# Performance work log

Hardware: AMD Instinct MI355X
Metric: run time of the kernel (lower is better)

The kernel has to match this reference:

```python
import jax, jax.numpy as jnp
import numpy as np
import math

B = 1; SEQ = 2048; CHUNK = 16; K = SEQ // CHUNK
DIM = 1024; NH = 16; HD = DIM // NH
NL = 2; NLF = 2; HID = 4096; VOCAB = 32000; CSP_MAX = 4
EPS = 1e-5
BS = CHUNK + 2                 # per-chunk decoder block: [fx, sep, tokens]
L = K * BS + 2                 # + trailing [fx_last, sep]


def rope_cache(n_pos, n_elem, base=10000.0):
    theta = 1.0 / (base ** (jnp.arange(0, n_elem, 2, dtype=jnp.float32) / n_elem))
    idx = jnp.outer(jnp.arange(n_pos, dtype=jnp.float32), theta)  # [n_pos, n_elem/2]
    cos = jnp.concatenate([jnp.cos(idx), jnp.cos(idx)], -1)
    sin = jnp.concatenate([jnp.sin(idx), jnp.sin(idx)], -1)
    return cos, sin  # [n_pos, n_elem]


def apply_rope(x, cos, sin):
    # x: [b, h, l, d]; cos/sin: [l, d] (rope_n_elem == head_dim)
    h = x.shape[-1] // 2
    rot = jnp.concatenate([-x[..., h:], x[..., :h]], -1)
    return x * cos + rot * sin


def rmsnorm(x, w):
    return x * jax.lax.rsqrt(jnp.mean(x * x, -1, keepdims=True) + EPS) * w


def attention(x, wqkv, wo, cos, sin, mask):
    b, l, d = x.shape
    qkv = (x @ wqkv).reshape(b, l, 3, NH, HD).transpose(2, 0, 3, 1, 4)
    q, k, v = qkv[0], qkv[1], qkv[2]            # [b, h, l, hd]
    q = apply_rope(q, cos, sin)
    k = apply_rope(k, cos, sin)
    s = jnp.einsum('bhqd,bhkd->bhqk', q, k) / math.sqrt(HD)
    if mask is not None:
        s = jnp.where(mask, s, jnp.float32(-1e30))
    o = jnp.einsum('bhqk,bhkd->bhqd', jax.nn.softmax(s, -1), v)
    return o.transpose(0, 2, 1, 3).reshape(b, l, d) @ wo


def block(x, ln1, wqkv, wo, ln2, wg, wu, wd, cos, sin, mask):
    x = x + attention(rmsnorm(x, ln1), wqkv, wo, cos, sin, mask)
    h = rmsnorm(x, ln2)
    return x + (jax.nn.silu(h @ wg) * (h @ wu)) @ wd


def cat_mask(n, bs):
    # CAT mask: (kv divides block-start | same block) & causal
    q = jnp.arange(n)[:, None]
    kv = jnp.arange(n)[None, :]
    return ((kv % bs == 0) | (q // bs == kv // bs)) & (q >= kv)


def setup_inputs() -> dict:
    key = jax.random.key(0)
    ks = jax.random.split(key, 24)
    w = lambda k, s: jax.random.normal(k, s, jnp.float32) * 0.02
    return {
        'input_ids': jax.random.randint(ks[0], (B, SEQ), 0, VOCAB, dtype=jnp.int32),
        'chunk_size_power': 4,
        'f_wte': w(ks[1], (VOCAB, DIM)), 'f_pos': w(ks[2], (SEQ, DIM)),
        'f_adapt': w(ks[3], (CSP_MAX + 1, DIM)),
        'f_ln1': jnp.ones((NLF, DIM)), 'f_ln2': jnp.ones((NLF, DIM)),
        'f_wqkv': w(ks[4], (NLF, DIM, 3 * DIM)), 'f_wo': w(ks[5], (NLF, DIM, DIM)),
        'f_wg': w(ks[6], (NLF, DIM, HID)), 'f_wu': w(ks[7], (NLF, DIM, HID)),
        'f_wd': w(ks[8], (NLF, HID, DIM)),
        'f_norm': jnp.ones((DIM,)), 'f_proj': w(ks[9], (DIM, CHUNK * DIM)),
        'dummy_fx': w(ks[10], (CSP_MAX + 1, DIM)), 'wte': w(ks[11], (VOCAB, DIM)),
        'sep': w(ks[12], (1, DIM)),
        'd_ln1': jnp.ones((NL, DIM)), 'd_ln2': jnp.ones((NL, DIM)),
        'd_wqkv': w(ks[13], (NL, DIM, 3 * DIM)), 'd_wo': w(ks[14], (NL, DIM, DIM)),
        'd_wg': w(ks[15], (NL, DIM, HID)), 'd_wu': w(ks[16], (NL, DIM, HID)),
        'd_wd': w(ks[17], (NL, HID, DIM)),
        'd_norm': jnp.ones((DIM,)), 'w_out': w(ks[18], (VOCAB, DIM)),
    }


def reference(input_ids, chunk_size_power, f_wte, f_pos, f_adapt, f_ln1, f_ln2,
              f_wqkv, f_wo, f_wg, f_wu, f_wd, f_norm, f_proj, dummy_fx, wte, sep,
              d_ln1, d_ln2, d_wqkv, d_wo, d_wg, d_wu, d_wd, d_norm, w_out):
    csp = int(chunk_size_power)
    ids = input_ids.reshape(B, K, CHUNK)
    cosf, sinf = rope_cache(2 + CHUNK, HD)

    def compress(ids_c, chunk_idx):
        # ids_c: [B, CHUNK] (one chunk, vmapped over K)
        x = f_wte[ids_c]
        adaptive = jnp.broadcast_to(f_adapt[csp], (B, 1, DIM))
        pos_tok = jnp.broadcast_to(f_pos[chunk_idx], (B, 1, DIM))
        x = jnp.concatenate([adaptive, pos_tok, x], 1)  # [B, CHUNK+2, DIM]
        for i in range(NLF):
            x = block(x, f_ln1[i], f_wqkv[i], f_wo[i], f_ln2[i],
                      f_wg[i], f_wu[i], f_wd[i], cosf, sinf, None)
        x = rmsnorm(x, f_norm)[:, 2:, :].reshape(B, CHUNK * DIM)
        # chunk_size_power == log2(CHUNK): bilinear interpolate to same size == identity
        return x @ f_proj.T  # [B, DIM]

    fx = jax.vmap(compress, in_axes=(1, 0), out_axes=1)(ids, jnp.arange(K))  # [B, K, DIM]

    fx_last = fx[:, -1:, :]
    dummy = jnp.broadcast_to(dummy_fx[csp], (B, 1, DIM))
    fx_sh = jnp.concatenate([dummy, fx[:, :-1, :]], 1)[:, :, None, :]  # [B, K, 1, DIM]
    sep_t = jnp.broadcast_to(sep[0], (B, K, 1, DIM))
    emb = wte[ids]  # [B, K, CHUNK, DIM]
    x = jnp.concatenate([fx_sh, sep_t, emb], 2).reshape(B, K * BS, DIM)
    x = jnp.concatenate([x, fx_last, jnp.broadcast_to(sep[0], (B, 1, DIM))], 1)  # [B, L, DIM]

    # per-block repeating RoPE positions (cache built for len BS, tiled)
    pos = jnp.tile(jnp.arange(BS), K + 1)[:L]
    cosb, sinb = rope_cache(BS, HD)
    cosd, sind = cosb[pos], sinb[pos]
    mask = cat_mask(L, BS)

    for i in range(NL):
        x = block(x, d_ln1[i], d_wqkv[i], d_wo[i], d_ln2[i],
                  d_wg[i], d_wu[i], d_wd[i], cosd, sind, mask)
    x = rmsnorm(x, d_norm)
    return x @ w_out.T  # [B, L, VOCAB]
```

## Files before the change

### kernel.cpp

```cpp
#include <hip/hip_runtime.h>
#include <math.h>

#define L_DEC 2306
#define MPAD 2560
#define T_FINE 2304

typedef float f32x4 __attribute__((ext_vector_type(4)));
typedef __bf16 bf16x8 __attribute__((ext_vector_type(8)));
typedef unsigned short u16;
typedef unsigned short us4 __attribute__((ext_vector_type(4)));
typedef unsigned short us8 __attribute__((ext_vector_type(8)));

#define GLOAD16(g, l) __builtin_amdgcn_global_load_lds( \
    (const __attribute__((address_space(1))) unsigned int*)(g), \
    (__attribute__((address_space(3))) unsigned int*)(l), 16, 0, 0)

__device__ __forceinline__ u16 f2bf(float f) {
  unsigned u = __float_as_uint(f);
  u += 0x7fffu + ((u >> 16) & 1u);
  return (u16)(u >> 16);
}

__device__ __forceinline__ int fix_csp(const int* p) {
  int c = p[0];
  if ((unsigned)c <= 4u) return c;
  float f = __uint_as_float((unsigned)c);
  int c2 = (int)f;
  return ((unsigned)c2 <= 4u) ? c2 : 4;
}

template<int ROWMAJ>
__device__ __forceinline__ void xcd_map(int gx, int gy, int& bm, int& bn, int TS) {
  const int nwg = gx * gy;
  const int orig = blockIdx.y * gx + blockIdx.x;
  const int q8 = nwg >> 3, r8 = nwg & 7;
  const int xcd = orig & 7, idx8 = orig >> 3;
  const int wg = (xcd < r8 ? xcd * (q8 + 1) : r8 * (q8 + 1) + (xcd - r8) * q8) + idx8;
  if (ROWMAJ) { bm = (wg / gx) * TS; bn = (wg % gx) * TS; }
  else        { bm = (wg % gy) * TS; bn = (wg / gy) * TS; }
}

template<int EPI>
__global__ __launch_bounds__(512, 1) void k_gemm3(const u16* __restrict__ A,
                                                  const u16* __restrict__ B,
                                                  float* __restrict__ C,
                                                  int N, int K, int Mstore)
{
  extern __shared__ u16 lds[];
  const int tid = threadIdx.x;
  int bm, bn; xcd_map<0>(gridDim.x, gridDim.y, bm, bn, 256);
  const int w = tid >> 6, lane = tid & 63;
  const int wm = (w >> 2) * 128, wn = (w & 3) * 64;
  const int lr = lane & 15, kh = lane >> 4;

#define STAGE3(buf, kt) do {                                                   \
    u16* lA = lds + (buf) * 32768;                                             \
    u16* lB = lA + 16384;                                                      \
    _Pragma("unroll")                                                          \
    for (int p = 0; p < 4; ++p) {                                              \
      int e = p * 512 + tid;                                                   \
      int row = e >> 3;                                                        \
      int kc = ((e & 7) ^ (row & 7)) * 8;    \
      GLOAD16(A + (size_t)(bm + row) * K + (size_t)(kt) * 64 + kc, lA + e * 8);\
      GLOAD16(B + (size_t)(bn + row) * K + (size_t)(kt) * 64 + kc, lB + e * 8);\
    }                                                                          \
  } while (0)

  f32x4 acc[8][4] = {};
  const int nt = K >> 6;
  STAGE3(0, 0);
  __syncthreads();
  int cur = 0;
  for (int t = 0; t < nt; ++t) {
    if (t + 1 < nt) STAGE3(cur ^ 1, t + 1);
    const u16* pA = lds + cur * 32768;
    const u16* pB = pA + 16384;
    const int xr = (lr & 7) << 3;
#pragma unroll
    for (int kt2 = 0; kt2 < 2; ++kt2) {
      bf16x8 af[8], bf[4];
#pragma unroll
      for (int m = 0; m < 8; ++m)
        af[m] = *(const bf16x8*)&pA[(wm + m * 16 + lr) * 64 + ((kt2 * 32 + kh * 8) ^ xr)];
#pragma unroll
      for (int n = 0; n < 4; ++n)
        bf[n] = *(const bf16x8*)&pB[(wn + n * 16 + lr) * 64 + ((kt2 * 32 + kh * 8) ^ xr)];
#pragma unroll
      for (int m = 0; m < 8; ++m)
#pragma unroll
        for (int n = 0; n < 4; ++n)
          acc[m][n] = __builtin_amdgcn_mfma_f32_16x16x32_bf16(af[m], bf[n], acc[m][n], 0, 0, 0);
    }
    __syncthreads();
    cur ^= 1;
  }
#undef STAGE3

#pragma unroll
  for (int m = 0; m < 8; ++m) {
    int gr0 = bm + wm + m * 16 + kh * 4;
#pragma unroll
    for (int n = 0; n < 4; ++n) {
      int gc = bn + wn + n * 16 + lr;
#pragma unroll
      for (int r = 0; r < 4; ++r) {
        int gr = gr0 + r;
        if (gr < Mstore) C[(size_t)gr * N + gc] = acc[m][n][r];
      }
    }
  }
}

template<int EPI>
__global__ __launch_bounds__(512, 1) void k_gemm2(const u16* __restrict__ A,
                                                  const u16* __restrict__ B,
                                                  float* __restrict__ C,
                                                  u16* __restrict__ Cb,
                                                  int N, int K, int Mstore)
{
  __shared__ u16 As[2][8192];
  __shared__ u16 Bs[2][8192];
  const int tid = threadIdx.x;
  int bm, bn; xcd_map<1>(gridDim.x, gridDim.y, bm, bn, 256);
  const int w = tid >> 6, lane = tid & 63;
  const int wm = (w >> 2) * 128, wn = (w & 3) * 64;
  const int lr = lane & 15, kh = lane >> 4;
  const int r0 = tid >> 2;
  const int ksrc = 8 * ((tid & 3) ^ ((tid >> 3) & 3));
  const u16* ga = A + (size_t)(bm + r0) * K + ksrc;
  const u16* gb = B + (size_t)(bn + r0) * K + ksrc;
  const size_t rstep = (size_t)128 * K;
  const int cola = (kh * 8) ^ (((lr >> 1) & 3) << 3);

#define STAGE2(buf, kt) do {                                   \
    const u16* gA = ga + (size_t)(kt) * 32;                    \
    const u16* gB = gb + (size_t)(kt) * 32;                    \
    GLOAD16(gA,         &As[buf][tid * 8]);                    \
    GLOAD16(gA + rstep, &As[buf][tid * 8 + 4096]);             \
    GLOAD16(gB,         &Bs[buf][tid * 8]);                    \
    GLOAD16(gB + rstep, &Bs[buf][tid * 8 + 4096]);             \
  } while (0)

  f32x4 acc[8][4] = {};
  const int nt = K >> 5;
  STAGE2(0, 0);
  __syncthreads();
  int cur = 0;
  for (int t = 0; t < nt; ++t) {
    if (t + 1 < nt) STAGE2(cur ^ 1, t + 1);
    bf16x8 af[8], bf[4];
#pragma unroll
    for (int m = 0; m < 8; ++m)
      af[m] = *(const bf16x8*)&As[cur][(wm + m * 16 + lr) * 32 + cola];
#pragma unroll
    for (int n = 0; n < 4; ++n)
      bf[n] = *(const bf16x8*)&Bs[cur][(wn + n * 16 + lr) * 32 + cola];
#pragma unroll
    for (int m = 0; m < 8; ++m)
#pragma unroll
      for (int n = 0; n < 4; ++n)
        acc[m][n] = __builtin_amdgcn_mfma_f32_16x16x32_bf16(af[m], bf[n], acc[m][n], 0, 0, 0);
    __syncthreads();
    cur ^= 1;
  }
#undef STAGE2

#pragma unroll
  for (int m = 0; m < 8; ++m) {
    int gr0 = bm + wm + m * 16 + kh * 4;
#pragma unroll
    for (int n = 0; n < 4; ++n) {
      int gc = bn + wn + n * 16 + lr;
#pragma unroll
      for (int r = 0; r < 4; ++r) {
        int gr = gr0 + r;
        if (gr < Mstore) C[(size_t)gr * N + gc] = acc[m][n][r];
      }
    }
  }
}

template<int EPI>
__global__ __launch_bounds__(256) void k_gemm_bt(const u16* __restrict__ A,
                                                 const u16* __restrict__ B,
                                                 float* __restrict__ C,
                                                 u16* __restrict__ Cb,
                                                 const float* __restrict__ cosT,
                                                 const float* __restrict__ sinT,
                                                 int N, int K, int Mstore, int kchunk)
{
  __shared__ u16 As[4096];
  __shared__ u16 Bs[4096];
  const int tid = threadIdx.x;
  int bm, bn; xcd_map<1>(gridDim.x, gridDim.y, bm, bn, 128);
  const int k0 = blockIdx.z * kchunk;
  const int w = tid >> 6, lane = tid & 63;
  const int wm = (w >> 1) * 64, wn = (w & 1) * 64;
  const int lr = lane & 15, kh = lane >> 4;
  const int r0 = tid >> 2;
  const int ksrc = 8 * ((tid & 3) ^ ((tid >> 3) & 3));
  const int cola = (kh * 8) ^ (((lr >> 1) & 3) << 3);

  const u16* ga = A + (size_t)(bm + r0) * K + k0 + ksrc;
  const u16* gb = B + (size_t)(bn + r0) * K + k0 + ksrc;
  u16* la = &As[tid * 8];
  u16* lb = &Bs[tid * 8];
  const size_t rstep = (size_t)64 * K;

  f32x4 acc[4][4] = {};
  for (int kk = 0; kk < kchunk; kk += 32) {
    GLOAD16(ga, la); GLOAD16(ga + rstep, la + 2048);
    GLOAD16(gb, lb); GLOAD16(gb + rstep, lb + 2048);
    ga += 32; gb += 32;
    __syncthreads();
    bf16x8 af[4], bfr[4];
#pragma unroll
    for (int m = 0; m < 4; ++m)
      af[m] = *(const bf16x8*)&As[(wm + m * 16 + lr) * 32 + cola];
#pragma unroll
    for (int n = 0; n < 4; ++n)
      bfr[n] = *(const bf16x8*)&Bs[(wn + n * 16 + lr) * 32 + cola];
#pragma unroll
    for (int m = 0; m < 4; ++m)
#pragma unroll
      for (int n = 0; n < 4; ++n)
        acc[m][n] = __builtin_amdgcn_mfma_f32_16x16x32_bf16(af[m], bfr[n], acc[m][n], 0, 0, 0);
    __syncthreads();
  }

  float* Cz = (EPI == 0) ? C + (size_t)blockIdx.z * Mstore * N : C;
  const int N2 = N >> 1;
  const bool doRope = (EPI == 3) && ((bn + wn) < 2048);
#pragma unroll
  for (int m = 0; m < 4; ++m) {
    int gr0 = bm + wm + m * 16 + kh * 4;
#pragma unroll
    for (int r = 0; r < 4; ++r) {
      int gr = gr0 + r;
      if (EPI == 3) {
        int p = gr % 18;
        if (doRope) {
#pragma unroll
          for (int n2 = 0; n2 < 2; ++n2) {
            int d = n2 * 16 + lr;
            float c = cosT[p * 64 + d], s = sinT[p * 64 + d];
            float x1 = acc[m][n2][r], x2 = acc[m][n2 + 2][r];
            if (gr < Mstore) {
              int gc = bn + wn + n2 * 16 + lr;
              C[(size_t)gr * N + gc]      = x1 * c - x2 * s;
              C[(size_t)gr * N + gc + 32] = x2 * c + x1 * s;
            }
          }
        } else if (gr < Mstore) {
#pragma unroll
          for (int n = 0; n < 4; ++n)
            C[(size_t)gr * N + bn + wn + n * 16 + lr] = acc[m][n][r];
        }
      } else if (EPI == 2) {
#pragma unroll
        for (int n = 0; n < 4; ++n) {
          float x = acc[m][n][r];
          float px = __shfl_xor(x, 1);
          if (!(lr & 1) && gr < Mstore) {
            int gc = bn + wn + n * 16 + lr;
            float sgl = x / (1.f + expf(-x)) * px;
            Cb[(size_t)gr * N2 + (gc >> 1)] = f2bf(sgl);
          }
        }
      } else {
        if (gr < Mstore) {
#pragma unroll
          for (int n = 0; n < 4; ++n) {
            size_t off = (size_t)gr * N + bn + wn + n * 16 + lr;
            if (EPI == 0) Cz[off] = acc[m][n][r];
            else          C[off] += acc[m][n][r];
          }
        }
      }
    }
  }
}

__global__ __launch_bounds__(256) void k_gemm_hf(const u16* __restrict__ A,
                                                 const float* __restrict__ B,
                                                 float* __restrict__ C,
                                                 int N, int K, int Mstore)
{
  __shared__ u16 As[4096];
  __shared__ u16 Bs[4096];
  const int tid = threadIdx.x;
  const int bm = blockIdx.y * 128, bn = blockIdx.x * 128;
  const int w = tid >> 6, lane = tid & 63;
  const int wm = (w >> 1) * 64, wn = (w & 1) * 64;
  const int lr = lane & 15, kh = lane >> 4;
  const int r0 = tid >> 2;
  const int ksrc = 8 * ((tid & 3) ^ ((tid >> 3) & 3));
  const int cola = (kh * 8) ^ (((lr >> 1) & 3) << 3);
  const u16* ga = A + (size_t)(bm + r0) * K + ksrc;
  u16* la = &As[tid * 8];
  const size_t rstep = (size_t)64 * K;

  f32x4 acc[4][4] = {};
  for (int kk = 0; kk < K; kk += 32) {
    GLOAD16(ga, la); GLOAD16(ga + rstep, la + 2048);
    ga += 32;
#pragma unroll
    for (int p = 0; p < 4; ++p) {
      int e = tid + p * 256;
      int row = e >> 3, kc = (e & 7) * 4;
      int kcs = kc ^ (((row >> 1) & 3) << 3);
      float4 v = *(const float4*)(B + (size_t)(bn + row) * K + kk + kc);
      us4 pk; pk[0] = f2bf(v.x); pk[1] = f2bf(v.y); pk[2] = f2bf(v.z); pk[3] = f2bf(v.w);
      *(us4*)&Bs[row * 32 + kcs] = pk;
    }
    __syncthreads();
    bf16x8 af[4], bfr[4];
#pragma unroll
    for (int m = 0; m < 4; ++m)
      af[m] = *(const bf16x8*)&As[(wm + m * 16 + lr) * 32 + cola];
#pragma unroll
    for (int n = 0; n < 4; ++n)
      bfr[n] = *(const bf16x8*)&Bs[(wn + n * 16 + lr) * 32 + cola];
#pragma unroll
    for (int m = 0; m < 4; ++m)
#pragma unroll
      for (int n = 0; n < 4; ++n)
        acc[m][n] = __builtin_amdgcn_mfma_f32_16x16x32_bf16(af[m], bfr[n], acc[m][n], 0, 0, 0);
    __syncthreads();
  }
#pragma unroll
  for (int m = 0; m < 4; ++m) {
    int gr0 = bm + wm + m * 16 + kh * 4;
#pragma unroll
    for (int n = 0; n < 4; ++n) {
      int gc = bn + wn + n * 16 + lr;
#pragma unroll
      for (int r = 0; r < 4; ++r) {
        int gr = gr0 + r;
        if (gr < Mstore) C[(size_t)gr * N + gc] = acc[m][n][r];
      }
    }
  }
}

__global__ __launch_bounds__(256) void k_wt2(const float* __restrict__ W,
                                             const float* __restrict__ W2,
                                             u16* __restrict__ Wt,
                                             int K, int N, int rs, int ro) {
  __shared__ u16 t[64][80];
  const float* src = (blockIdx.z == 0) ? W : W2;
  int roz = ro + blockIdx.z;
  int n0 = blockIdx.x * 64, k0 = blockIdx.y * 64;
#pragma unroll
  for (int p = 0; p < 4; ++p) {
    int id = threadIdx.x + p * 256;
    int row = id >> 4, c4 = (id & 15) * 4;
    float4 v = *(const float4*)(src + (size_t)(k0 + row) * N + n0 + c4);
    t[c4 + 0][row] = f2bf(v.x);
    t[c4 + 1][row] = f2bf(v.y);
    t[c4 + 2][row] = f2bf(v.z);
    t[c4 + 3][row] = f2bf(v.w);
  }
  __syncthreads();
#pragma unroll
  for (int p = 0; p < 2; ++p) {
    int id = threadIdx.x + p * 256;
    int row = id >> 3, c8 = (id & 7) * 8;
    *(us8*)(Wt + ((size_t)(n0 + row) * rs + roz) * K + k0 + c8) = *(const us8*)&t[row][c8];
  }
}

__global__ void k_cvt(const float* __restrict__ x, u16* __restrict__ y, int n4) {
  for (int i = blockIdx.x * 256 + threadIdx.x; i < n4; i += gridDim.x * 256) {
    float4 v = ((const float4*)x)[i];
    us4 p; p[0] = f2bf(v.x); p[1] = f2bf(v.y); p[2] = f2bf(v.z); p[3] = f2bf(v.w);
    ((us4*)y)[i] = p;
  }
}

__global__ void k_reduce_add(const float* __restrict__ p, float* __restrict__ dst,
                             int n, int planes, int addDst) {
  for (int i = blockIdx.x * 256 + threadIdx.x; i < n; i += gridDim.x * 256) {
    float s = addDst ? dst[i] : 0.f;
    for (int z = 0; z < planes; ++z) s += p[(size_t)z * n + i];
    dst[i] = s;
  }
}

template<int S, int NORM>
__global__ __launch_bounds__(256) void k_red_norm(const float* __restrict__ planes,
                                                  float* __restrict__ x,
                                                  const float* __restrict__ w,
                                                  u16* __restrict__ y) {
  const int t = blockIdx.x;
  const int n = gridDim.x * 1024;
  const size_t base = (size_t)t * 1024 + threadIdx.x * 4;
  float4 a = *(const float4*)(x + base);
#pragma unroll
  for (int s = 0; s < S; ++s) {
    float4 p = *(const float4*)(planes + (size_t)s * n + base);
    a.x += p.x; a.y += p.y; a.z += p.z; a.w += p.w;
  }
  *(float4*)(x + base) = a;
  if (NORM) {
    float ss = a.x * a.x + a.y * a.y + a.z * a.z + a.w * a.w;
#pragma unroll
    for (int off = 32; off; off >>= 1) ss += __shfl_xor(ss, off);
    __shared__ float ps[4];
    if ((threadIdx.x & 63) == 0) ps[threadIdx.x >> 6] = ss;
    __syncthreads();
    float inv = rsqrtf((ps[0] + ps[1] + ps[2] + ps[3]) * (1.f / 1024.f) + 1e-5f);
    const float4 wv = *(const float4*)(w + threadIdx.x * 4);
    us4 o;
    o[0] = f2bf(a.x * inv * wv.x); o[1] = f2bf(a.y * inv * wv.y);
    o[2] = f2bf(a.z * inv * wv.z); o[3] = f2bf(a.w * inv * wv.w);
    *(us4*)(y + base) = o;
  }
}

__global__ void k_rope_table(float* __restrict__ cosT, float* __restrict__ sinT) {
  int i = blockIdx.x * blockDim.x + threadIdx.x;
  if (i >= 18 * 64) return;
  int p = i >> 6, d = i & 63;
  float theta = powf(10000.f, -(float)(d & 31) / 32.f);
  float ang = (float)p * theta;
  cosT[i] = cosf(ang);
  sinT[i] = sinf(ang);
}

__global__ void k_fine_embed(const int* __restrict__ ids, const int* __restrict__ cspp,
                             const float* __restrict__ f_wte, const float* __restrict__ f_pos,
                             const float* __restrict__ f_adapt, float* __restrict__ xF) {
  int csp = fix_csp(cspp);
  for (int idx = blockIdx.x * 256 + threadIdx.x; idx < T_FINE * 1024; idx += gridDim.x * 256) {
    int r = idx >> 10, d = idx & 1023;
    int c = r / 18, j = r - c * 18;
    float v;
    if (j == 0)      v = f_adapt[csp * 1024 + d];
    else if (j == 1) v = f_pos[c * 1024 + d];
    else             v = f_wte[(size_t)ids[c * 16 + j - 2] * 1024 + d];
    xF[idx] = v;
  }
}

__global__ __launch_bounds__(256) void k_rmsnorm_bf(const float* __restrict__ x,
                                                    const float* __restrict__ w,
                                                    u16* __restrict__ y) {
  int t = blockIdx.x;
  const float4 v = *(const float4*)(x + (size_t)t * 1024 + threadIdx.x * 4);
  float ss = v.x * v.x + v.y * v.y + v.z * v.z + v.w * v.w;
#pragma unroll
  for (int off = 32; off; off >>= 1) ss += __shfl_xor(ss, off);
  __shared__ float ps[4];
  if ((threadIdx.x & 63) == 0) ps[threadIdx.x >> 6] = ss;
  __syncthreads();
  float inv = rsqrtf((ps[0] + ps[1] + ps[2] + ps[3]) * (1.f / 1024.f) + 1e-5f);
  const float4 wv = *(const float4*)(w + threadIdx.x * 4);
  us4 o;
  o[0] = f2bf(v.x * inv * wv.x); o[1] = f2bf(v.y * inv * wv.y);
  o[2] = f2bf(v.z * inv * wv.z); o[3] = f2bf(v.w * inv * wv.w);
  *(us4*)(y + (size_t)t * 1024 + threadIdx.x * 4) = o;
}

__global__ __launch_bounds__(256) void k_rmsnorm_pack_bf(const float* __restrict__ x,
                                                         const float* __restrict__ w,
                                                         u16* __restrict__ y) {
  int b = blockIdx.x;
  int c = b >> 4, r = b & 15;
  const float* xr = x + (size_t)(c * 18 + 2 + r) * 1024;
  const float4 v = *(const float4*)(xr + threadIdx.x * 4);
  float ss = v.x * v.x + v.y * v.y + v.z * v.z + v.w * v.w;
#pragma unroll
  for (int off = 32; off; off >>= 1) ss += __shfl_xor(ss, off);
  __shared__ float ps[4];
  if ((threadIdx.x & 63) == 0) ps[threadIdx.x >> 6] = ss;
  __syncthreads();
  float inv = rsqrtf((ps[0] + ps[1] + ps[2] + ps[3]) * (1.f / 1024.f) + 1e-5f);
  const float4 wv = *(const float4*)(w + threadIdx.x * 4);
  us4 o;
  o[0] = f2bf(v.x * inv * wv.x); o[1] = f2bf(v.y * inv * wv.y);
  o[2] = f2bf(v.z * inv * wv.z); o[3] = f2bf(v.w * inv * wv.w);
  *(us4*)(y + (size_t)b * 1024 + threadIdx.x * 4) = o;
}

__global__ __launch_bounds__(256) void k_attn_fine2(const float* __restrict__ qkv,
                                                    u16* __restrict__ out) {
  __shared__ float q[4][18][68], k[4][18][68], v[4][18][68], s[4][18][20];
  int c = blockIdx.x;
  int w = threadIdx.x >> 6, lane = threadIdx.x & 63;
  int h = blockIdx.y * 4 + w;
  const float* base = qkv + (size_t)c * 18 * 3072 + h * 64;
#pragma unroll 3
  for (int r = 0; r < 18; ++r) {
    q[w][r][lane] = base[(size_t)r * 3072 + lane];
    k[w][r][lane] = base[(size_t)r * 3072 + 1024 + lane];
    v[w][r][lane] = base[(size_t)r * 3072 + 2048 + lane];
  }
  __syncthreads();
#pragma unroll
  for (int it = 0; it < 6; ++it) {
    int idx = lane + it * 64;
    if (idx < 324) {
      int qi = (idx * 3641) >> 16;
      int ki = idx - qi * 18;
      const float* qr = q[w][qi];
      const float* kr = k[w][ki];
      float a = 0.f;
#pragma unroll
      for (int d = 0; d < 64; d += 4) {
        float4 x = *(const float4*)&qr[d];
        float4 y = *(const float4*)&kr[d];
        a += x.x * y.x + x.y * y.y + x.z * y.z + x.w * y.w;
      }
      s[w][qi][ki] = a * 0.125f;
    }
  }
  __syncthreads();
  if (lane < 18) {
    float mx = -1e30f;
#pragma unroll
    for (int j = 0; j < 18; ++j) mx = fmaxf(mx, s[w][lane][j]);
    float sum = 0.f;
#pragma unroll
    for (int j = 0; j < 18; ++j) { float e = expf(s[w][lane][j] - mx); s[w][lane][j] = e; sum += e; }
    float inv = 1.f / sum;
#pragma unroll
    for (int j = 0; j < 18; ++j) s[w][lane][j] *= inv;
  }
  __syncthreads();
  float vcol[18];
#pragma unroll
  for (int ki = 0; ki < 18; ++ki) vcol[ki] = v[w][ki][lane];
#pragma unroll 2
  for (int qi = 0; qi < 18; ++qi) {
    float o = 0.f;
#pragma unroll
    for (int ki = 0; ki < 18; ++ki) o += s[w][qi][ki] * vcol[ki];
    out[(size_t)(c * 18 + qi) * 1024 + h * 64 + lane] = f2bf(o);
  }
}

__global__ __launch_bounds__(512) void k_attn_dec3(const float* __restrict__ qkv,
                                                   u16* __restrict__ out) {
  extern __shared__ float dyn[];
  float* Kl = dyn;
  float* Vl = Kl + 146 * 65;
  float* Ql = Vl + 146 * 65;
  float* Sw = Ql + 18 * 65;
  const int bq = blockIdx.x, h = blockIdx.y;
  const int w = threadIdx.x >> 6, lane = threadIdx.x & 63;
  const int t0 = 18 * bq;
  const int nq = (bq < 128) ? 18 : 2;
  const int nstage = (bq < 128) ? (bq + 18) : 130;

  {
    int rr = threadIdx.x >> 2, c = threadIdx.x & 3;
    for (int row = rr; row < nstage; row += 128) {
      int kv = (row <= bq) ? 18 * row : t0 + (row - bq);
      const float* kp = qkv + (size_t)kv * 3072 + 1024 + h * 64 + c * 16;
#pragma unroll
      for (int q4 = 0; q4 < 4; ++q4) {
        float4 a = *(const float4*)(kp + q4 * 4);
        float4 b = *(const float4*)(kp + 1024 + q4 * 4);
        int d = c * 16 + q4 * 4;
        float* kd = Kl + row * 65 + d;
        float* vd = Vl + row * 65 + d;
        kd[0] = a.x; kd[1] = a.y; kd[2] = a.z; kd[3] = a.w;
        vd[0] = b.x; vd[1] = b.y; vd[2] = b.z; vd[3] = b.w;
      }
    }
    if (rr < nq) {
      const float* qp = qkv + (size_t)(t0 + rr) * 3072 + h * 64 + c * 16;
#pragma unroll
      for (int q4 = 0; q4 < 4; ++q4) {
        float4 a = *(const float4*)(qp + q4 * 4);
        int d = c * 16 + q4 * 4;
        float* qd = Ql + rr * 65 + d;
        qd[0] = a.x; qd[1] = a.y; qd[2] = a.z; qd[3] = a.w;
      }
    }
  }
  __syncthreads();

  for (int r = w; r < nq; r += 8) {
    const int nk = bq + 1 + r;
    float* S = Sw + w * 148;
    const float* qr = Ql + r * 65;
    float mx = -1e30f;
    for (int i = lane; i < nk; i += 64) {
      const float* kr = Kl + i * 65;
      float a = 0.f;
#pragma unroll
      for (int d = 0; d < 64; ++d) a += qr[d] * kr[d];
      a *= 0.125f;
      S[i] = a;
      mx = fmaxf(mx, a);
    }
#pragma unroll
    for (int off = 32; off; off >>= 1) mx = fmaxf(mx, __shfl_xor(mx, off));
    float sum = 0.f;
    for (int i = lane; i < nk; i += 64) { float e = expf(S[i] - mx); S[i] = e; sum += e; }
#pragma unroll
    for (int off = 32; off; off >>= 1) sum += __shfl_xor(sum, off);
    float inv = 1.f / sum;
    __builtin_amdgcn_wave_barrier();
    float o = 0.f;
    for (int i = 0; i < nk; ++i) o += S[i] * Vl[i * 65 + lane];
    out[(size_t)(t0 + r) * 1024 + h * 64 + lane] = f2bf(o * inv);
  }
}

__global__ __launch_bounds__(256) void k_attn_dec2(const float* __restrict__ qkv,
                                                   u16* __restrict__ out) {
  __shared__ float sc_s[4][160];
  int t = blockIdx.x;
  int w = threadIdx.x >> 6, lane = threadIdx.x & 63;
  int h = blockIdx.y * 4 + w;
  float* sc = sc_s[w];
  int bq = t / 18;
  int nstart = bq + 1;
  int nown = t - 18 * bq;
  int nk = nstart + nown;
  int g = lane >> 2, j = lane & 3;
  const float* qb = qkv + (size_t)t * 3072 + h * 64 + j * 16;
  float4 q0 = *(const float4*)(qb);
  float4 q1 = *(const float4*)(qb + 4);
  float4 q2 = *(const float4*)(qb + 8);
  float4 q3 = *(const float4*)(qb + 12);
  for (int i0 = 0; i0 < nk; i0 += 16) {
    int i = i0 + g;
    float p = 0.f;
    if (i < nk) {
      int kv = (i < nstart) ? 18 * i : 18 * bq + (i - nstart) + 1;
      const float* kp = qkv + (size_t)kv * 3072 + 1024 + h * 64 + j * 16;
      float4 k0 = *(const float4*)(kp);
      float4 k1 = *(const float4*)(kp + 4);
      float4 k2 = *(const float4*)(kp + 8);
      float4 k3 = *(const float4*)(kp + 12);
      p = q0.x * k0.x + q0.y * k0.y + q0.z * k0.z + q0.w * k0.w
        + q1.x * k1.x + q1.y * k1.y + q1.z * k1.z + q1.w * k1.w
        + q2.x * k2.x + q2.y * k2.y + q2.z * k2.z + q2.w * k2.w
        + q3.x * k3.x + q3.y * k3.y + q3.z * k3.z + q3.w * k3.w;
    }
    p += __shfl_xor(p, 1);
    p += __shfl_xor(p, 2);
    if (i < nk && j == 0) sc[i] = p * 0.125f;
  }
  __syncthreads();
  float mx = -1e30f;
  for (int i = lane; i < nk; i += 64) mx = fmaxf(mx, sc[i]);
#pragma unroll
  for (int off = 32; off; off >>= 1) mx = fmaxf(mx, __shfl_xor(mx, off));
  float sum = 0.f;
  for (int i = lane; i < nk; i += 64) { float e = expf(sc[i] - mx); sc[i] = e; sum += e; }
#pragma unroll
  for (int off = 32; off; off >>= 1) sum += __shfl_xor(sum, off);
  float inv = 1.f / sum;
  __syncthreads();
  const float* vb = qkv + 2048 + h * 64 + lane;
  float o0 = 0.f, o1 = 0.f, o2 = 0.f, o3 = 0.f;
  int i = 0;
  for (; i + 4 <= nk; i += 4) {
    int ia = i, ib = i + 1, ic = i + 2, id = i + 3;
    int kva = (ia < nstart) ? 18 * ia : 18 * bq + (ia - nstart) + 1;
    int kvb = (ib < nstart) ? 18 * ib : 18 * bq + (ib - nstart) + 1;
    int kvc = (ic < nstart) ? 18 * ic : 18 * bq + (ic - nstart) + 1;
    int kvd = (id < nstart) ? 18 * id : 18 * bq + (id - nstart) + 1;
    o0 += sc[ia] * vb[(size_t)kva * 3072];
    o1 += sc[ib] * vb[(size_t)kvb * 3072];
    o2 += sc[ic] * vb[(size_t)kvc * 3072];
    o3 += sc[id] * vb[(size_t)kvd * 3072];
  }
  for (; i < nk; ++i) {
    int kv = (i < nstart) ? 18 * i : 18 * bq + (i - nstart) + 1;
    o0 += sc[i] * vb[(size_t)kv * 3072];
  }
  float o = (o0 + o1) + (o2 + o3);
  out[(size_t)t * 1024 + h * 64 + lane] = f2bf(o * inv);
}

__global__ void k_assemble(const int* __restrict__ ids, const int* __restrict__ cspp,
                           const float* __restrict__ fx, const float* __restrict__ dummy_fx,
                           const float* __restrict__ sep, const float* __restrict__ wte,
                           float* __restrict__ xD) {
  int csp = fix_csp(cspp);
  for (int idx = blockIdx.x * 256 + threadIdx.x; idx < MPAD * 1024; idx += gridDim.x * 256) {
    int t = idx >> 10, d = idx & 1023;
    float v;
    if (t >= L_DEC)     v = 0.f;
    else if (t == 2305) v = sep[d];
    else if (t == 2304) v = fx[127 * 1024 + d];
    else {
      int k = t / 18, r = t - k * 18;
      if (r == 0)      v = (k == 0) ? dummy_fx[csp * 1024 + d] : fx[(k - 1) * 1024 + d];
      else if (r == 1) v = sep[d];
      else             v = wte[(size_t)ids[k * 16 + r - 2] * 1024 + d];
    }
    xD[idx] = v;
  }
}

extern "C" void kernel_launch(void* const* d_in, const int* in_sizes, int n_in,
                              void* d_out, int out_size, void* d_ws, size_t ws_size,
                              hipStream_t stream) {
  const int*   input_ids = (const int*)d_in[0];
  const int*   cspp      = (const int*)d_in[1];
  const float* f_wte     = (const float*)d_in[2];
  const float* f_pos     = (const float*)d_in[3];
  const float* f_adapt   = (const float*)d_in[4];
  const float* f_ln1     = (const float*)d_in[5];
  const float* f_ln2     = (const float*)d_in[6];
  const float* f_wqkv    = (const float*)d_in[7];
  const float* f_wo      = (const float*)d_in[8];
  const float* f_wg      = (const float*)d_in[9];
  const float* f_wu      = (const float*)d_in[10];
  const float* f_wd      = (const float*)d_in[11];
  const float* f_norm    = (const float*)d_in[12];
  const float* f_proj    = (const float*)d_in[13];
  const float* dummy_fx  = (const float*)d_in[14];
  const float* wte       = (const float*)d_in[15];
  const float* sep       = (const float*)d_in[16];
  const float* d_ln1     = (const float*)d_in[17];
  const float* d_ln2     = (const float*)d_in[18];
  const float* d_wqkv    = (const float*)d_in[19];
  const float* d_wo      = (const float*)d_in[20];
  const float* d_wg      = (const float*)d_in[21];
  const float* d_wu      = (const float*)d_in[22];
  const float* d_wd      = (const float*)d_in[23];
  const float* d_norm    = (const float*)d_in[24];
  const float* w_out     = (const float*)d_in[25];

  float* cosT = (float*)d_ws;
  float* sinT = cosT + 1152;
  u16*   bufH = (u16*)(sinT + 1152);
  u16*   w_outb = bufH + (size_t)MPAD * 1024;
  const size_t WS_NEED = 2 * 1152 * 4 + (size_t)MPAD * 1024 * 2 + (size_t)32000 * 1024 * 2;
  const bool big_ws = ws_size >= WS_NEED;

  float* o       = (float*)d_out;
  float* xF      = o;
  float* xD      = xF + (size_t)T_FINE * 1024;
  float* fx      = xD + (size_t)MPAD * 1024;
  float* bufQKV  = fx + 128 * 1024;
  u16*   bufA    = (u16*)(bufQKV + (size_t)MPAD * 3072);
  u16*   bufGb   = bufA + (size_t)MPAD * 1024;
  u16*   packedb = bufGb + (size_t)MPAD * 4096;
  u16*   Wt      = packedb + (size_t)128 * 16384;
  u16*   projb   = Wt + (size_t)8192 * 1024;
  float* spk     = (float*)(projb + (size_t)1024 * 16384);

  const size_t ATTN_LDS = (size_t)(146 * 65 * 2 + 18 * 65 + 8 * 148) * 4;
  hipError_t eattn = hipFuncSetAttribute(
      reinterpret_cast<const void*>(&k_attn_dec3),
      hipFuncAttributeMaxDynamicSharedMemorySize, (int)ATTN_LDS);

#define GEMM_BT(EPI, Ap, Bp, Cp, Cbp, Mpad, N, K, Mstore, S) \
  k_gemm_bt<EPI><<<dim3((N) / 128, (Mpad) / 128, (S)), 256, 0, stream>>>((Ap), (Bp), (Cp), (Cbp), cosT, sinT, (N), (K), (Mstore), (K) / (S))
#define WT1(Wp, Kd, Nd) k_wt2<<<dim3((Nd) / 64, (Kd) / 64, 1), 256, 0, stream>>>((Wp), nullptr, Wt, (Kd), (Nd), 1, 0)

  k_rope_table<<<5, 256, 0, stream>>>(cosT, sinT);
  k_fine_embed<<<2048, 256, 0, stream>>>(input_ids, cspp, f_wte, f_pos, f_adapt, xF);
  k_rmsnorm_bf<<<T_FINE, 256, 0, stream>>>(xF, f_ln1, bufH);

  for (int i = 0; i < 2; ++i) {
    WT1(f_wqkv + (size_t)i * 1024 * 3072, 1024, 3072);
    GEMM_BT(3, bufH, Wt, bufQKV, (u16*)nullptr, T_FINE, 3072, 1024, T_FINE, 1);
    k_attn_fine2<<<dim3(128, 4), 256, 0, stream>>>(bufQKV, bufA);
    WT1(f_wo + (size_t)i * 1024 * 1024, 1024, 1024);
    GEMM_BT(0, bufA, Wt, spk, (u16*)nullptr, T_FINE, 1024, 1024, T_FINE, 2);
    k_red_norm<2, 1><<<T_FINE, 256, 0, stream>>>(spk, xF, f_ln2 + i * 1024, bufH);
    k_wt2<<<dim3(64, 16, 2), 256, 0, stream>>>(f_wg + (size_t)i * 1024 * 4096,
                                               f_wu + (size_t)i * 1024 * 4096, Wt, 1024, 4096, 2, 0);
    GEMM_BT(2, bufH, Wt, (float*)nullptr, bufGb, T_FINE, 8192, 1024, T_FINE, 1);
    WT1(f_wd + (size_t)i * 4096 * 1024, 4096, 1024);
    GEMM_BT(0, bufGb, Wt, spk, (u16*)nullptr, T_FINE, 1024, 4096, T_FINE, 4);
    if (i == 0) k_red_norm<4, 1><<<T_FINE, 256, 0, stream>>>(spk, xF, f_ln1 + 1024, bufH);
    else        k_red_norm<4, 0><<<T_FINE, 256, 0, stream>>>(spk, xF, nullptr, nullptr);
  }

  k_rmsnorm_pack_bf<<<2048, 256, 0, stream>>>(xF, f_norm, packedb);
  k_cvt<<<2048, 256, 0, stream>>>(f_proj, projb, 1024 * 16384 / 4);
  GEMM_BT(0, packedb, projb, spk, (u16*)nullptr, 128, 1024, 16384, 128, 32);
  k_reduce_add<<<512, 256, 0, stream>>>(spk, fx, 128 * 1024, 32, 0);

  k_assemble<<<2048, 256, 0, stream>>>(input_ids, cspp, fx, dummy_fx, sep, wte, xD);
  k_rmsnorm_bf<<<MPAD, 256, 0, stream>>>(xD, d_ln1, bufH);
  for (int i = 0; i < 2; ++i) {
    WT1(d_wqkv + (size_t)i * 1024 * 3072, 1024, 3072);
    GEMM_BT(3, bufH, Wt, bufQKV, (u16*)nullptr, MPAD, 3072, 1024, MPAD, 1);
    if (eattn == hipSuccess) {
      k_attn_dec3<<<dim3(129, 16), 512, ATTN_LDS, stream>>>(bufQKV, bufA);
    } else {
      k_attn_dec2<<<dim3(L_DEC, 4), 256, 0, stream>>>(bufQKV, bufA);
    }
    WT1(d_wo + (size_t)i * 1024 * 1024, 1024, 1024);
    GEMM_BT(0, bufA, Wt, spk, (u16*)nullptr, MPAD, 1024, 1024, MPAD, 2);
    k_red_norm<2, 1><<<MPAD, 256, 0, stream>>>(spk, xD, d_ln2 + i * 1024, bufH);
    k_wt2<<<dim3(64, 16, 2), 256, 0, stream>>>(d_wg + (size_t)i * 1024 * 4096,
                                               d_wu + (size_t)i * 1024 * 4096, Wt, 1024, 4096, 2, 0);
    GEMM_BT(2, bufH, Wt, (float*)nullptr, bufGb, MPAD, 8192, 1024, MPAD, 1);
    WT1(d_wd + (size_t)i * 4096 * 1024, 4096, 1024);
    GEMM_BT(0, bufGb, Wt, spk, (u16*)nullptr, MPAD, 1024, 4096, MPAD, 4);
    const float* nw = (i == 0) ? d_ln1 + 1024 : d_norm;
    k_red_norm<4, 1><<<MPAD, 256, 0, stream>>>(spk, xD, nw, bufH);
  }

  if (big_ws) {
    k_cvt<<<2048, 256, 0, stream>>>(w_out, w_outb, 32000 * 1024 / 4);
    hipError_t ae = hipFuncSetAttribute(
        reinterpret_cast<const void*>(&k_gemm3<0>),
        hipFuncAttributeMaxDynamicSharedMemorySize, 131072);
    if (ae == hipSuccess) {
      k_gemm3<0><<<dim3(125, 10), 512, 131072, stream>>>(bufH, w_outb, o, 32000, 1024, L_DEC);
    } else {
      k_gemm2<0><<<dim3(125, 10), 512, 0, stream>>>(bufH, w_outb, o, nullptr, 32000, 1024, L_DEC);
    }
  } else {
    k_gemm_hf<<<dim3(250, MPAD / 128), 256, 0, stream>>>(bufH, w_out, o, 32000, 1024, L_DEC);
  }
#undef WT1
#undef GEMM_BT
}
```

Baseline: 1.387 ms.

## Double-buffer k_gemm_bt with 64-wide K tiles and unify XCD tile mapping

```diff
diff --git a/kernel.cpp b/kernel.cpp
--- a/kernel.cpp
+++ b/kernel.cpp
@@ -29,15 +29,14 @@
   return ((unsigned)c2 <= 4u) ? c2 : 4;
 }
 
-template<int ROWMAJ>
 __device__ __forceinline__ void xcd_map(int gx, int gy, int& bm, int& bn, int TS) {
   const int nwg = gx * gy;
   const int orig = blockIdx.y * gx + blockIdx.x;
   const int q8 = nwg >> 3, r8 = nwg & 7;
   const int xcd = orig & 7, idx8 = orig >> 3;
   const int wg = (xcd < r8 ? xcd * (q8 + 1) : r8 * (q8 + 1) + (xcd - r8) * q8) + idx8;
-  if (ROWMAJ) { bm = (wg / gx) * TS; bn = (wg % gx) * TS; }
-  else        { bm = (wg % gy) * TS; bn = (wg / gy) * TS; }
+  bm = (wg / gx) * TS;
+  bn = (wg % gx) * TS;
 }
 
 template<int EPI>
@@ -48,7 +47,7 @@
 {
   extern __shared__ u16 lds[];
   const int tid = threadIdx.x;
-  int bm, bn; xcd_map<0>(gridDim.x, gridDim.y, bm, bn, 256);
+  int bm, bn; xcd_map(gridDim.x, gridDim.y, bm, bn, 256);
   const int w = tid >> 6, lane = tid & 63;
   const int wm = (w >> 2) * 128, wn = (w & 3) * 64;
   const int lr = lane & 15, kh = lane >> 4;
@@ -121,7 +120,7 @@
   __shared__ u16 As[2][8192];
   __shared__ u16 Bs[2][8192];
   const int tid = threadIdx.x;
-  int bm, bn; xcd_map<1>(gridDim.x, gridDim.y, bm, bn, 256);
+  int bm, bn; xcd_map(gridDim.x, gridDim.y, bm, bn, 256);
   const int w = tid >> 6, lane = tid & 63;
   const int wm = (w >> 2) * 128, wn = (w & 3) * 64;
   const int lr = lane & 15, kh = lane >> 4;
@@ -189,44 +188,59 @@
                                                  const float* __restrict__ sinT,
                                                  int N, int K, int Mstore, int kchunk)
 {
-  __shared__ u16 As[4096];
-  __shared__ u16 Bs[4096];
+  __shared__ u16 As[2][4096];
+  __shared__ u16 Bs[2][4096];
   const int tid = threadIdx.x;
-  int bm, bn; xcd_map<1>(gridDim.x, gridDim.y, bm, bn, 128);
+  int bm, bn; xcd_map(gridDim.x, gridDim.y, bm, bn, 128);
   const int k0 = blockIdx.z * kchunk;
   const int w = tid >> 6, lane = tid & 63;
   const int wm = (w >> 1) * 64, wn = (w & 1) * 64;
   const int lr = lane & 15, kh = lane >> 4;
-  const int r0 = tid >> 2;
-  const int ksrc = 8 * ((tid & 3) ^ ((tid >> 3) & 3));
-  const int cola = (kh * 8) ^ (((lr >> 1) & 3) << 3);
-
-  const u16* ga = A + (size_t)(bm + r0) * K + k0 + ksrc;
-  const u16* gb = B + (size_t)(bn + r0) * K + k0 + ksrc;
-  u16* la = &As[tid * 8];
-  u16* lb = &Bs[tid * 8];
-  const size_t rstep = (size_t)64 * K;
+  (void)As; (void)Bs;
+  __shared__ u16 ldsAB[2][16384];
+
+#define STAGE4(buf, kt) do {                                                       \
+    u16* lA = &ldsAB[buf][0];                                                      \
+    u16* lB = &ldsAB[buf][8192];                                                   \
+    _Pragma("unroll")                                                              \
+    for (int p = 0; p < 4; ++p) {                                                  \
+      int e = p * 256 + tid;                                                       \
+      int row = e >> 3;                                                            \
+      int kc = ((e & 7) ^ (row & 7)) * 8;                                          \
+      GLOAD16(A + (size_t)(bm + row) * K + k0 + (size_t)(kt) * 64 + kc, lA + e * 8);\
+      GLOAD16(B + (size_t)(bn + row) * K + k0 + (size_t)(kt) * 64 + kc, lB + e * 8);\
+    }                                                                              \
+  } while (0)
 
   f32x4 acc[4][4] = {};
-  for (int kk = 0; kk < kchunk; kk += 32) {
-    GLOAD16(ga, la); GLOAD16(ga + rstep, la + 2048);
-    GLOAD16(gb, lb); GLOAD16(gb + rstep, lb + 2048);
-    ga += 32; gb += 32;
+  const int nt = kchunk >> 6;
+  STAGE4(0, 0);
+  __syncthreads();
+  int cur = 0;
+  for (int t = 0; t < nt; ++t) {
+    if (t + 1 < nt) STAGE4(cur ^ 1, t + 1);
+    const u16* pA = &ldsAB[cur][0];
+    const u16* pB = &ldsAB[cur][8192];
+    const int xr = (lr & 7) << 3;
+#pragma unroll
+    for (int kt2 = 0; kt2 < 2; ++kt2) {
+      bf16x8 af[4], bfr[4];
+#pragma unroll
+      for (int m = 0; m < 4; ++m)
+        af[m] = *(const bf16x8*)&pA[(wm + m * 16 + lr) * 64 + ((kt2 * 32 + kh * 8) ^ xr)];
+#pragma unroll
+      for (int n = 0; n < 4; ++n)
+        bfr[n] = *(const bf16x8*)&pB[(wn + n * 16 + lr) * 64 + ((kt2 * 32 + kh * 8) ^ xr)];
+#pragma unroll
+      for (int m = 0; m < 4; ++m)
+#pragma unroll
+        for (int n = 0; n < 4; ++n)
+          acc[m][n] = __builtin_amdgcn_mfma_f32_16x16x32_bf16(af[m], bfr[n], acc[m][n], 0, 0, 0);
+    }
     __syncthreads();
-    bf16x8 af[4], bfr[4];
-#pragma unroll
-    for (int m = 0; m < 4; ++m)
-      af[m] = *(const bf16x8*)&As[(wm + m * 16 + lr) * 32 + cola];
-#pragma unroll
-    for (int n = 0; n < 4; ++n)
-      bfr[n] = *(const bf16x8*)&Bs[(wn + n * 16 + lr) * 32 + cola];
-#pragma unroll
-    for (int m = 0; m < 4; ++m)
-#pragma unroll
-      for (int n = 0; n < 4; ++n)
-        acc[m][n] = __builtin_amdgcn_mfma_f32_16x16x32_bf16(af[m], bfr[n], acc[m][n], 0, 0, 0);
-    __syncthreads();
-  }
+    cur ^= 1;
+  }
+#undef STAGE4
 
   float* Cz = (EPI == 0) ? C + (size_t)blockIdx.z * Mstore * N : C;
   const int N2 = N >> 1;
@@ -270,11 +284,8 @@
       } else {
         if (gr < Mstore) {
 #pragma unroll
-          for (int n = 0; n < 4; ++n) {
-            size_t off = (size_t)gr * N + bn + wn + n * 16 + lr;
-            if (EPI == 0) Cz[off] = acc[m][n][r];
-            else          C[off] += acc[m][n][r];
-          }
+          for (int n = 0; n < 4; ++n)
+            Cz[(size_t)gr * N + bn + wn + n * 16 + lr] = acc[m][n][r];
         }
       }
     }
```

New measurement: 1.292 ms. 1.07x faster.
